# Kernel optimization log

Measured on AMD Instinct MI355X. Metric: run time of the kernel, lower is better.

The kernel has to match this reference:

```python
import jax, jax.numpy as jnp
import numpy as np

N_NODES = 50000
N_EDGES = 262144
HID = 256
N_CLS = 2


def setup_inputs() -> dict:
    key = jax.random.key(0)
    ks = jax.random.split(key, 6)
    node_repr = jax.random.normal(ks[0], (N_NODES, HID), dtype=jnp.float32)
    src = jax.random.randint(ks[1], (N_EDGES,), 0, N_NODES, dtype=jnp.int64)
    dst = jax.random.randint(ks[2], (N_EDGES,), 0, N_NODES, dtype=jnp.int64)
    # Linear weights stored as (in, out); init ~ torch default scale
    W1 = jax.random.normal(ks[3], (4 * HID, 2 * HID), dtype=jnp.float32) * (1.0 / np.sqrt(4 * HID))
    b1 = jnp.zeros((2 * HID,), dtype=jnp.float32)
    W2 = jax.random.normal(ks[4], (2 * HID, N_CLS), dtype=jnp.float32) * (1.0 / np.sqrt(2 * HID))
    b2 = jnp.zeros((N_CLS,), dtype=jnp.float32)
    return {"node_repr": node_repr, "src": src, "dst": dst,
            "W1": W1, "b1": b1, "W2": W2, "b2": b2}


def reference(node_repr, src, dst, W1, b1, W2, b2):
    h_i = node_repr[src]                      # [E, H] gather
    h_j = node_repr[dst]                      # [E, H] gather
    edge_input = jnp.concatenate(
        [h_i, h_j, jnp.abs(h_i - h_j), h_i * h_j], axis=1)  # [E, 4H]
    h = jax.nn.relu(edge_input @ W1 + b1)     # [E, 2H]; dropout = identity (eval)
    return h @ W2 + b2                        # [E, C]
```

## Files before the change

### kernel.cpp

```cpp
#include <hip/hip_runtime.h>

#define N_NODES 50000
#define E_EDGES 262144

typedef __attribute__((ext_vector_type(8))) _Float16 f16x8;
typedef __attribute__((ext_vector_type(2))) _Float16 f16x2;
typedef __attribute__((ext_vector_type(4))) float f32x4;

union V16 { uint4 u; f16x8 h; };
union U32 { unsigned u; f16x2 p; };

__device__ __forceinline__ unsigned h2pack(float a, float b) {
  union { _Float16 h[2]; unsigned u; } r;
  r.h[0] = (_Float16)a;
  r.h[1] = (_Float16)b;
  return r.u;
}
__device__ __forceinline__ void async_gather16(const void* gptr, void* lptr) {
  __builtin_amdgcn_global_load_lds(
      (const __attribute__((address_space(1))) void*)gptr,
      (__attribute__((address_space(3))) void*)lptr, 16, 0, 0);
}

__global__ void cvt_node_kernel(const float* __restrict__ x, unsigned short* __restrict__ y) {
  int i = (blockIdx.x * 256 + threadIdx.x) * 8;
  float4 f0 = *(const float4*)(x + i);
  float4 f1 = *(const float4*)(x + i + 4);
  uint4 o;
  o.x = h2pack(f0.x, f0.y);
  o.y = h2pack(f0.z, f0.w);
  o.z = h2pack(f1.x, f1.y);
  o.w = h2pack(f1.z, f1.w);
  *(uint4*)(y + i) = o;
}

__global__ void prep_w1pp2_kernel(const float* __restrict__ w1, unsigned short* __restrict__ w1pp2) {
  int t = blockIdx.x * 256 + threadIdx.x;
  int step = t >> 13;
  int rem = t & 8191;
  int sq = rem >> 9;
  int col = rem & 511;
  int s = sq >> 2, qd = sq & 3;
  int k0 = s * 256 + step * 32 + qd * 8;
  float f[8];
#pragma unroll
  for (int i = 0; i < 8; ++i) f[i] = w1[(size_t)(k0 + i) * 512 + col];
  uint4 o;
  o.x = h2pack(f[0], f[1]);
  o.y = h2pack(f[2], f[3]);
  o.z = h2pack(f[4], f[5]);
  o.w = h2pack(f[6], f[7]);
  *(uint4*)(w1pp2 + (size_t)t * 8) = o;
}

__global__ void init_out_kernel(float* __restrict__ out, const float* __restrict__ b2) {
  int i = blockIdx.x * 256 + threadIdx.x;
  float2 v; v.x = b2[0]; v.y = b2[1];
  *(float2*)(out + (size_t)i * 2) = v;
}

__global__ __launch_bounds__(256) void edge_mlp_kernel(
    const unsigned short* __restrict__ nodeb,
    const unsigned short* __restrict__ w1pp2,
    const int* __restrict__ src,
    const int* __restrict__ dst,
    const float* __restrict__ b1,
    const float* __restrict__ w2,
    float* __restrict__ out) {
  __shared__ char smem[65536];

  const int tid = threadIdx.x;
  const int wid = tid >> 6;
  const int lane = tid & 63;
  const int quad = lane >> 4;
  const int l16 = lane & 15;
  const int bx = blockIdx.x;
  const int xc = bx & 7;
  const int t2 = bx >> 3;
  const int n_half = t2 & 1;
  const int m_idx = (t2 >> 1) * 8 + xc;
  const int row0 = m_idx * 64;
  const int n0 = n_half * 256 + wid * 64;

  const char* nodeB = (const char*)nodeb;
  const char* w1B = (const char*)w1pp2;

  unsigned bOff[4];
#pragma unroll
  for (int s = 0; s < 4; ++s)
    bOff[s] = (unsigned)((s * 4 + quad) * 8192 + (n0 + l16) * 16);
  const char* w1s = w1B;

  const unsigned aXor = (unsigned)(l16 & 7);
  const unsigned aBase = (unsigned)(l16 * 512);

  f32x4 acc[4][4];
#pragma unroll
  for (int mt = 0; mt < 4; ++mt)
#pragma unroll
    for (int nt = 0; nt < 4; ++nt)
      acc[mt][nt] = (f32x4){0.f, 0.f, 0.f, 0.f};

  {
    const int eh = tid >> 5;
    const unsigned wsw = (unsigned)(((tid & 31) ^ (eh & 7)) << 4);
#pragma unroll
    for (int c = 0; c < 8; ++c) {
      int e = c * 8 + eh;
      unsigned so = ((unsigned)src[row0 + e] << 9) + wsw;
      unsigned do_ = ((unsigned)dst[row0 + e] << 9) + wsw;
      async_gather16(nodeB + so, smem + c * 4096 + wid * 1024);
      async_gather16(nodeB + do_, smem + 32768 + c * 4096 + wid * 1024);
    }
  }
  __syncthreads();

#pragma unroll 2
  for (int step = 0; step < 8; ++step) {
    V16 bf[4][4];
#pragma unroll
    for (int s = 0; s < 4; ++s)
#pragma unroll
      for (int nt = 0; nt < 4; ++nt)
        bf[s][nt].u = *(const uint4*)(w1s + bOff[s] + nt * 256);
    const unsigned stq = (unsigned)(step * 4 + quad);
    V16 hi[4], hj[4];
#pragma unroll
    for (int mt = 0; mt < 4; ++mt) {
      unsigned ao = (unsigned)(mt * 16 * 512) + aBase + ((stq ^ aXor) << 4);
      hi[mt].u = *(const uint4*)(smem + ao);
      hj[mt].u = *(const uint4*)(smem + 32768 + ao);
    }
#pragma unroll
    for (int sl = 0; sl < 2; ++sl) {
#pragma unroll
      for (int mt = 0; mt < 4; ++mt) {
        f16x8 af = (sl == 0) ? hi[mt].h : hj[mt].h;
#pragma unroll
        for (int nt = 0; nt < 4; ++nt)
          acc[mt][nt] = __builtin_amdgcn_mfma_f32_16x16x32_f16(af, bf[sl][nt].h, acc[mt][nt], 0, 0, 0);
      }
    }
#pragma unroll
    for (int mt = 0; mt < 4; ++mt) {
      const unsigned hw[4] = {hi[mt].u.x, hi[mt].u.y, hi[mt].u.z, hi[mt].u.w};
      const unsigned jw[4] = {hj[mt].u.x, hj[mt].u.y, hj[mt].u.z, hj[mt].u.w};
      unsigned d[4], pr[4];
#pragma unroll
      for (int w = 0; w < 4; ++w) {
        U32 hx, jx, dd, pp;
        hx.u = hw[w];
        jx.u = jw[w];
        dd.p = hx.p - jx.p;
        d[w] = dd.u & 0x7fff7fffu;
        pp.p = hx.p * jx.p;
        pr[w] = pp.u;
      }
      V16 a2, a3;
      a2.u = make_uint4(d[0], d[1], d[2], d[3]);
      a3.u = make_uint4(pr[0], pr[1], pr[2], pr[3]);
#pragma unroll
      for (int nt = 0; nt < 4; ++nt)
        acc[mt][nt] = __builtin_amdgcn_mfma_f32_16x16x32_f16(a2.h, bf[2][nt].h, acc[mt][nt], 0, 0, 0);
#pragma unroll
      for (int nt = 0; nt < 4; ++nt)
        acc[mt][nt] = __builtin_amdgcn_mfma_f32_16x16x32_f16(a3.h, bf[3][nt].h, acc[mt][nt], 0, 0, 0);
    }
    w1s += 131072;
  }

#pragma unroll
  for (int mt = 0; mt < 4; ++mt) {
    float pc0[4] = {0.f, 0.f, 0.f, 0.f};
    float pc1[4] = {0.f, 0.f, 0.f, 0.f};
#pragma unroll
    for (int nt = 0; nt < 4; ++nt) {
      int gc = n0 + nt * 16 + l16;
      float b1v = b1[gc];
      float w20 = w2[gc * 2 + 0];
      float w21 = w2[gc * 2 + 1];
#pragma unroll
      for (int r = 0; r < 4; ++r) {
        float v = fmaxf(acc[mt][nt][r] + b1v, 0.f);
        pc0[r] = fmaf(v, w20, pc0[r]);
        pc1[r] = fmaf(v, w21, pc1[r]);
      }
    }
#pragma unroll
    for (int r = 0; r < 4; ++r) {
      float s0 = pc0[r], s1 = pc1[r];
#pragma unroll
      for (int off = 1; off < 16; off <<= 1) {
        s0 += __shfl_xor(s0, off);
        s1 += __shfl_xor(s1, off);
      }
      int e = row0 + mt * 16 + quad * 4 + r;
      if (l16 == 0) unsafeAtomicAdd(&out[(size_t)e * 2 + 0], s0);
      if (l16 == 1) unsafeAtomicAdd(&out[(size_t)e * 2 + 1], s1);
    }
  }
}

extern "C" void kernel_launch(void* const* d_in, const int* in_sizes, int n_in,
                              void* d_out, int out_size, void* d_ws, size_t ws_size,
                              hipStream_t stream) {
  const float* node = (const float*)d_in[0];
  const int* src = (const int*)d_in[1];
  const int* dst = (const int*)d_in[2];
  const float* W1 = (const float*)d_in[3];
  const float* b1 = (const float*)d_in[4];
  const float* W2 = (const float*)d_in[5];
  const float* b2 = (const float*)d_in[6];
  float* out = (float*)d_out;

  unsigned short* nodeb = (unsigned short*)d_ws;
  unsigned short* w1pp2 = (unsigned short*)((char*)d_ws + 25600000);

  cvt_node_kernel<<<6250, 256, 0, stream>>>(node, nodeb);
  prep_w1pp2_kernel<<<256, 256, 0, stream>>>(W1, w1pp2);
  init_out_kernel<<<1024, 256, 0, stream>>>(out, b2);
  edge_mlp_kernel<<<8192, 256, 0, stream>>>(nodeb, w1pp2, src, dst, b1, W2, out);
}
```

Baseline: 417.0 us.

## Split N into quarters and stage gathered rows in two K-chunks to halve LDS

Each block now computes a quarter of the hidden columns (32 per wave) instead of half, doubling the grid. The gathered src/dst rows are staged in two 256-byte chunks with a barrier between them, halving LDS per block to 32KB and shrinking the accumulator set. The aim is higher occupancy and lower register pressure. The cost is that every edge row is gathered twice as often across blocks, plus extra barriers inside each block.

```diff
diff --git a/kernel.cpp b/kernel.cpp
--- a/kernel.cpp
+++ b/kernel.cpp
@@ -67,7 +67,7 @@
     const float* __restrict__ b1,
     const float* __restrict__ w2,
     float* __restrict__ out) {
-  __shared__ char smem[65536];
+  __shared__ char smem[32768];
 
   const int tid = threadIdx.x;
   const int wid = tid >> 6;
@@ -77,10 +77,10 @@
   const int bx = blockIdx.x;
   const int xc = bx & 7;
   const int t2 = bx >> 3;
-  const int n_half = t2 & 1;
-  const int m_idx = (t2 >> 1) * 8 + xc;
+  const int n_quarter = t2 & 3;
+  const int m_idx = (t2 >> 2) * 8 + xc;
   const int row0 = m_idx * 64;
-  const int n0 = n_half * 256 + wid * 64;
+  const int n0 = n_quarter * 128 + wid * 32;
 
   const char* nodeB = (const char*)nodeb;
   const char* w1B = (const char*)w1pp2;
@@ -92,55 +92,53 @@
   const char* w1s = w1B;
 
   const unsigned aXor = (unsigned)(l16 & 7);
-  const unsigned aBase = (unsigned)(l16 * 512);
-
-  f32x4 acc[4][4];
+  const unsigned aBase = (unsigned)(l16 * 256);
+
+  f32x4 acc[4][2];
 #pragma unroll
   for (int mt = 0; mt < 4; ++mt)
 #pragma unroll
-    for (int nt = 0; nt < 4; ++nt)
+    for (int nt = 0; nt < 2; ++nt)
       acc[mt][nt] = (f32x4){0.f, 0.f, 0.f, 0.f};
 
-  {
-    const int eh = tid >> 5;
-    const unsigned wsw = (unsigned)(((tid & 31) ^ (eh & 7)) << 4);
-#pragma unroll
-    for (int c = 0; c < 8; ++c) {
-      int e = c * 8 + eh;
+  auto stage_chunk = [&](int ck) {
+    const int eh = tid >> 4;
+    const unsigned wsw = (unsigned)(((tid & 15) ^ (eh & 7)) << 4) + (unsigned)(ck * 256);
+#pragma unroll
+    for (int c = 0; c < 4; ++c) {
+      int e = c * 16 + eh;
       unsigned so = ((unsigned)src[row0 + e] << 9) + wsw;
       unsigned do_ = ((unsigned)dst[row0 + e] << 9) + wsw;
       async_gather16(nodeB + so, smem + c * 4096 + wid * 1024);
-      async_gather16(nodeB + do_, smem + 32768 + c * 4096 + wid * 1024);
-    }
-  }
-  __syncthreads();
-
-#pragma unroll 2
-  for (int step = 0; step < 8; ++step) {
-    V16 bf[4][4];
+      async_gather16(nodeB + do_, smem + 16384 + c * 4096 + wid * 1024);
+    }
+  };
+
+  auto kstep = [&](int st4) {
+    V16 bf[4][2];
 #pragma unroll
     for (int s = 0; s < 4; ++s)
 #pragma unroll
-      for (int nt = 0; nt < 4; ++nt)
+      for (int nt = 0; nt < 2; ++nt)
         bf[s][nt].u = *(const uint4*)(w1s + bOff[s] + nt * 256);
-    const unsigned stq = (unsigned)(step * 4 + quad);
+    const unsigned stq = (unsigned)(st4 * 4 + quad);
     V16 hi[4], hj[4];
 #pragma unroll
     for (int mt = 0; mt < 4; ++mt) {
-      unsigned ao = (unsigned)(mt * 16 * 512) + aBase + ((stq ^ aXor) << 4);
+      unsigned ao = (unsigned)(mt * 16 * 256) + aBase + ((stq ^ aXor) << 4);
       hi[mt].u = *(const uint4*)(smem + ao);
-      hj[mt].u = *(const uint4*)(smem + 32768 + ao);
-    }
-#pragma unroll
-    for (int sl = 0; sl < 2; ++sl) {
-#pragma unroll
-      for (int mt = 0; mt < 4; ++mt) {
-        f16x8 af = (sl == 0) ? hi[mt].h : hj[mt].h;
-#pragma unroll
-        for (int nt = 0; nt < 4; ++nt)
-          acc[mt][nt] = __builtin_amdgcn_mfma_f32_16x16x32_f16(af, bf[sl][nt].h, acc[mt][nt], 0, 0, 0);
-      }
-    }
+      hj[mt].u = *(const uint4*)(smem + 16384 + ao);
+    }
+#pragma unroll
+    for (int mt = 0; mt < 4; ++mt)
+#pragma unroll
+      for (int nt = 0; nt < 2; ++nt)
+        acc[mt][nt] = __builtin_amdgcn_mfma_f32_16x16x32_f16(hi[mt].h, bf[0][nt].h, acc[mt][nt], 0, 0, 0);
+#pragma unroll
+    for (int mt = 0; mt < 4; ++mt)
+#pragma unroll
+      for (int nt = 0; nt < 2; ++nt)
+        acc[mt][nt] = __builtin_amdgcn_mfma_f32_16x16x32_f16(hj[mt].h, bf[1][nt].h, acc[mt][nt], 0, 0, 0);
 #pragma unroll
     for (int mt = 0; mt < 4; ++mt) {
       const unsigned hw[4] = {hi[mt].u.x, hi[mt].u.y, hi[mt].u.z, hi[mt].u.w};
@@ -160,21 +158,32 @@
       a2.u = make_uint4(d[0], d[1], d[2], d[3]);
       a3.u = make_uint4(pr[0], pr[1], pr[2], pr[3]);
 #pragma unroll
-      for (int nt = 0; nt < 4; ++nt)
+      for (int nt = 0; nt < 2; ++nt)
         acc[mt][nt] = __builtin_amdgcn_mfma_f32_16x16x32_f16(a2.h, bf[2][nt].h, acc[mt][nt], 0, 0, 0);
 #pragma unroll
-      for (int nt = 0; nt < 4; ++nt)
+      for (int nt = 0; nt < 2; ++nt)
         acc[mt][nt] = __builtin_amdgcn_mfma_f32_16x16x32_f16(a3.h, bf[3][nt].h, acc[mt][nt], 0, 0, 0);
     }
     w1s += 131072;
-  }
+  };
+
+  stage_chunk(0);
+  __syncthreads();
+#pragma unroll 2
+  for (int st4 = 0; st4 < 4; ++st4) kstep(st4);
+
+  __syncthreads();
+  stage_chunk(1);
+  __syncthreads();
+#pragma unroll 2
+  for (int st4 = 0; st4 < 4; ++st4) kstep(st4);
 
 #pragma unroll
   for (int mt = 0; mt < 4; ++mt) {
     float pc0[4] = {0.f, 0.f, 0.f, 0.f};
     float pc1[4] = {0.f, 0.f, 0.f, 0.f};
 #pragma unroll
-    for (int nt = 0; nt < 4; ++nt) {
+    for (int nt = 0; nt < 2; ++nt) {
       int gc = n0 + nt * 16 + l16;
       float b1v = b1[gc];
       float w20 = w2[gc * 2 + 0];
@@ -219,5 +228,5 @@
   cvt_node_kernel<<<6250, 256, 0, stream>>>(node, nodeb);
   prep_w1pp2_kernel<<<256, 256, 0, stream>>>(W1, w1pp2);
   init_out_kernel<<<1024, 256, 0, stream>>>(out, b2);
-  edge_mlp_kernel<<<8192, 256, 0, stream>>>(nodeb, w1pp2, src, dst, b1, W2, out);
-}
+  edge_mlp_kernel<<<16384, 256, 0, stream>>>(nodeb, w1pp2, src, dst, b1, W2, out);
+}
```

After: 532.3 us. 27.7% more time.
